# Kernel tuning notes

Measured on AMD Instinct MI355X. Metric: run time of the kernel, lower is better.

Reference implementation:

```python
import jax, jax.numpy as jnp
import numpy as np
from jax import lax

B, H, LQ, LF, V = 8, 12, 32, 256, 32000


def setup_inputs() -> dict:
    key = jax.random.key(0)
    k1, k2, k3 = jax.random.split(key, 3)
    return {
        "attention_scores": jax.random.normal(k1, (B, H, LQ, LF), jnp.float32),
        "q_logits": jax.random.normal(k2, (B, LQ, V), jnp.float32),
        "f_logits": jax.random.normal(k3, (B, LF, V), jnp.float32),
        "q_mask": jnp.ones((B, LQ), jnp.float32),
        "attention_mask": jnp.ones((B, LF), jnp.float32),
        "samples": 4,
    }


def reference(attention_scores, q_logits, f_logits, q_mask, attention_mask, samples):
    # attention_scores: [B,H,Lq,Lf] -> mean over heads, max over query positions
    scores = attention_scores.mean(axis=1)            # [B,Lq,Lf]
    aggregated = scores.max(axis=1)                   # [B,Lf]
    probs = jax.nn.sigmoid(aggregated) * attention_mask  # [B,Lf]

    # Bernoulli sampling for first samples-1 draws, deterministic threshold for the last
    skey = jax.random.key(42)
    sampled = jax.random.bernoulli(skey, probs, (samples - 1,) + probs.shape)
    last = (probs >= 0.5)[None]
    actions = jnp.concatenate([sampled, last], axis=0).astype(f_logits.dtype)  # [S,B,Lf]

    # Bernoulli log-prob summed over tokens: a*log(p) + (1-a)*log(1-p)
    logprobs = jnp.where(actions > 0.5, jnp.log(probs)[None], jnp.log1p(-probs)[None]).sum(-1)  # [S,B]

    # value = max over concat([q_logits, f_logits*action]) of log1p(relu(.)) * mask
    # Since action in {0,1}: log1p(relu(x*a)) = a * log1p(relu(x))
    lq = jnp.log1p(jax.nn.relu(q_logits)) * q_mask[:, :, None]   # [B,Lq,V]
    q_max = lq.max(axis=1)                                       # [B,V]
    lf = jnp.log1p(jax.nn.relu(f_logits))                        # [B,Lf,V]

    def step(carry, action):
        am = (action * attention_mask)[:, :, None]               # [B,Lf,1]
        f_val = (lf * am).max(axis=1)                            # [B,V]
        return carry, jnp.maximum(q_max, f_val)                  # masked max over concat dim

    _, values = lax.scan(step, None, actions)                    # [S,B,V]
    return values, logprobs, actions
```

## Files before the change

### kernel.cpp

```cpp
#include <hip/hip_runtime.h>
#include <stdint.h>

#define NB 8
#define NH 12
#define NLQ 32
#define NLF 256
#define NV 32000
#define NS 4
#define NV4 (NV / 4)

#define OUT_LOGP (NS * NB * NV)
#define OUT_ACT  (OUT_LOGP + NS * NB)

__device__ __forceinline__ uint32_t rotl32(uint32_t v, int r) {
  return (v << r) | (v >> (32 - r));
}

__device__ __forceinline__ void threefry2x32(uint32_t k0, uint32_t k1,
                                             uint32_t& x0, uint32_t& x1) {
  const uint32_t ks2 = k0 ^ k1 ^ 0x1BD11BDAu;
  x0 += k0; x1 += k1;
#define TF_ROUND(r) { x0 += x1; x1 = rotl32(x1, r); x1 ^= x0; }
  TF_ROUND(13) TF_ROUND(15) TF_ROUND(26) TF_ROUND(6)
  x0 += k1; x1 += ks2 + 1u;
  TF_ROUND(17) TF_ROUND(29) TF_ROUND(16) TF_ROUND(24)
  x0 += ks2; x1 += k0 + 2u;
  TF_ROUND(13) TF_ROUND(15) TF_ROUND(26) TF_ROUND(6)
  x0 += k0; x1 += k1 + 3u;
  TF_ROUND(17) TF_ROUND(29) TF_ROUND(16) TF_ROUND(24)
  x0 += k1; x1 += ks2 + 4u;
  TF_ROUND(13) TF_ROUND(15) TF_ROUND(26) TF_ROUND(6)
  x0 += ks2; x1 += k0 + 5u;
#undef TF_ROUND
}

__global__ __launch_bounds__(256) void k_mean(const float* __restrict__ as,
                                              float* __restrict__ scores) {
  const int o = blockIdx.x * 256 + threadIdx.x;
  const int f  = o & (NLF - 1);
  const int lq = (o >> 8) & (NLQ - 1);
  const int b  = o >> 13;
  float s = 0.f;
#pragma unroll
  for (int h = 0; h < NH; ++h)
    s += as[(((size_t)(b * NH + h) * NLQ) + lq) * NLF + f];
  scores[o] = s / 12.0f;
}

__global__ __launch_bounds__(256) void k_probs(
    const float* __restrict__ scores,
    const float* __restrict__ attn_mask,
    float* __restrict__ out,
    unsigned* __restrict__ actmask)
{
  const int b = blockIdx.x;
  const int f = threadIdx.x;

  float agg = -INFINITY;
#pragma unroll
  for (int lq = 0; lq < NLQ; ++lq)
    agg = fmaxf(agg, scores[(b * NLQ + lq) * NLF + f]);

  const float amask = attn_mask[b * NLF + f];
  const float p = amask * (1.0f / (1.0f + expf(-agg)));

  const float lp  = logf(p);
  const float l1p = log1pf(-p);

  unsigned mask = 0;
  float terms[NS];
#pragma unroll
  for (int s = 0; s < NS; ++s) {
    bool act;
    if (s < NS - 1) {
      const uint32_t n = (uint32_t)(s * (NB * NLF) + b * NLF + f);
      uint32_t x0 = 0u, x1 = n;
      threefry2x32(0u, 42u, x0, x1);
      const uint32_t bits = x0 ^ x1;
      const float u = __uint_as_float((bits >> 9) | 0x3f800000u) - 1.0f;
      act = (u < p);
    } else {
      act = (p >= 0.5f);
    }
    if (act) mask |= (1u << s);
    terms[s] = act ? lp : l1p;
    out[OUT_ACT + (s * NB + b) * NLF + f] = act ? 1.0f : 0.0f;
  }
  actmask[b * NLF + f] = mask;

  __shared__ float red[NS][NLF];
#pragma unroll
  for (int s = 0; s < NS; ++s) red[s][f] = terms[s];
  __syncthreads();
  for (int off = 128; off > 0; off >>= 1) {
    if (f < off) {
#pragma unroll
      for (int s = 0; s < NS; ++s) red[s][f] += red[s][f + off];
    }
    __syncthreads();
  }
  if (f == 0) {
#pragma unroll
    for (int s = 0; s < NS; ++s) out[OUT_LOGP + s * NB + b] = red[s][0];
  }
}

__global__ __launch_bounds__(256) void k_values(
    const float* __restrict__ q_logits,
    const float* __restrict__ f_logits,
    const float* __restrict__ q_mask,
    const unsigned* __restrict__ actmask,
    float* __restrict__ out)
{
  const int b = blockIdx.y;
  const int tid = threadIdx.x;

  __shared__ float ssel[NS][NLF];
  __shared__ float sqsel[NLQ];
  {
    const unsigned mk = actmask[b * NLF + tid];
#pragma unroll
    for (int s = 0; s < NS; ++s)
      ssel[s][tid] = (mk >> s) & 1u ? INFINITY : -INFINITY;
    if (tid < NLQ)
      sqsel[tid] = (q_mask[b * NLQ + tid] > 0.5f) ? INFINITY : -INFINITY;
  }
  __syncthreads();

  const int c4 = blockIdx.x * 256 + tid;
  if (c4 >= NV4) return;

  const float4* qp = (const float4*)q_logits;
  const float4* fp = (const float4*)f_logits;

  float4 qm4 = make_float4(-INFINITY, -INFINITY, -INFINITY, -INFINITY);
#pragma unroll
  for (int l0 = 0; l0 < NLQ; l0 += 8) {
    float4 x[8];
#pragma unroll
    for (int j = 0; j < 8; ++j)
      x[j] = qp[(size_t)(b * NLQ + l0 + j) * NV4 + c4];
#pragma unroll
    for (int j = 0; j < 8; ++j) {
      const float sv = sqsel[l0 + j];
      qm4.x = fmaxf(qm4.x, fminf(x[j].x, sv));
      qm4.y = fmaxf(qm4.y, fminf(x[j].y, sv));
      qm4.z = fmaxf(qm4.z, fminf(x[j].z, sv));
      qm4.w = fmaxf(qm4.w, fminf(x[j].w, sv));
    }
  }
  const float q0 = log1pf(fmaxf(qm4.x, 0.f));
  const float q1 = log1pf(fmaxf(qm4.y, 0.f));
  const float q2 = log1pf(fmaxf(qm4.z, 0.f));
  const float q3 = log1pf(fmaxf(qm4.w, 0.f));

  float m[NS][4];
#pragma unroll
  for (int s = 0; s < NS; ++s)
#pragma unroll
    for (int c = 0; c < 4; ++c) m[s][c] = -INFINITY;

  for (int f0 = 0; f0 < NLF; f0 += 8) {
    float4 x[8];
#pragma unroll
    for (int j = 0; j < 8; ++j)
      x[j] = fp[(size_t)(b * NLF + f0 + j) * NV4 + c4];
#pragma unroll
    for (int j = 0; j < 8; ++j) {
#pragma unroll
      for (int s = 0; s < NS; ++s) {
        const float sv = ssel[s][f0 + j];
        m[s][0] = fmaxf(m[s][0], fminf(x[j].x, sv));
        m[s][1] = fmaxf(m[s][1], fminf(x[j].y, sv));
        m[s][2] = fmaxf(m[s][2], fminf(x[j].z, sv));
        m[s][3] = fmaxf(m[s][3], fminf(x[j].w, sv));
      }
    }
  }

  float4* ov = (float4*)out;
#pragma unroll
  for (int s = 0; s < NS; ++s) {
    float4 r;
    r.x = fmaxf(q0, log1pf(fmaxf(m[s][0], 0.f)));
    r.y = fmaxf(q1, log1pf(fmaxf(m[s][1], 0.f)));
    r.z = fmaxf(q2, log1pf(fmaxf(m[s][2], 0.f)));
    r.w = fmaxf(q3, log1pf(fmaxf(m[s][3], 0.f)));
    ov[(size_t)(s * NB + b) * NV4 + c4] = r;
  }
}

extern "C" void kernel_launch(void* const* d_in, const int* in_sizes, int n_in,
                              void* d_out, int out_size, void* d_ws, size_t ws_size,
                              hipStream_t stream) {
  const float* attn_scores = (const float*)d_in[0];
  const float* q_logits    = (const float*)d_in[1];
  const float* f_logits    = (const float*)d_in[2];
  const float* q_mask      = (const float*)d_in[3];
  const float* attn_mask   = (const float*)d_in[4];
  float* out = (float*)d_out;

  float* ws_scores   = (float*)d_ws;
  unsigned* ws_mask  = (unsigned*)(ws_scores + NB * NLQ * NLF);

  k_mean<<<dim3((NB * NLQ * NLF) / 256), 256, 0, stream>>>(attn_scores, ws_scores);
  k_probs<<<dim3(NB), 256, 0, stream>>>(ws_scores, attn_mask, out, ws_mask);
  k_values<<<dim3((NV4 + 255) / 256, NB), 256, 0, stream>>>(
      q_logits, f_logits, q_mask, ws_mask, out);
}
```

Before: 388.7 us.

## Split the values reduction over token chunks and add a finalize max kernel

Splits the q/f token reduction in the values kernel into four chunks along a new grid dimension. Each chunk writes raw partial maxima to workspace, and a new finalize kernel combines them and applies log1p(relu). The goal is more blocks in flight to better saturate memory bandwidth. The cost is extra workspace traffic for the partials and one more kernel launch.

Result: slower. 396.9 us (+2.1%).

```diff
diff --git a/kernel.cpp b/kernel.cpp
--- a/kernel.cpp
+++ b/kernel.cpp
@@ -8,6 +8,10 @@
 #define NV 32000
 #define NS 4
 #define NV4 (NV / 4)
+
+#define PSPLIT 4
+#define FCHUNK (NLF / PSPLIT)
+#define QCHUNK (NLQ / PSPLIT)
 
 #define OUT_LOGP (NS * NB * NV)
 #define OUT_ACT  (OUT_LOGP + NS * NB)
@@ -105,26 +109,28 @@
   }
 }
 
-__global__ __launch_bounds__(256) void k_values(
+__global__ __launch_bounds__(256) void k_values_part(
     const float* __restrict__ q_logits,
     const float* __restrict__ f_logits,
     const float* __restrict__ q_mask,
     const unsigned* __restrict__ actmask,
-    float* __restrict__ out)
+    float* __restrict__ part)
 {
   const int b = blockIdx.y;
+  const int p = blockIdx.z;
   const int tid = threadIdx.x;
 
-  __shared__ float ssel[NS][NLF];
-  __shared__ float sqsel[NLQ];
-  {
-    const unsigned mk = actmask[b * NLF + tid];
+  __shared__ float ssel[NS][FCHUNK];
+  __shared__ float sqsel[QCHUNK];
+  if (tid < FCHUNK) {
+    const unsigned mk = actmask[b * NLF + p * FCHUNK + tid];
 #pragma unroll
     for (int s = 0; s < NS; ++s)
       ssel[s][tid] = (mk >> s) & 1u ? INFINITY : -INFINITY;
-    if (tid < NLQ)
-      sqsel[tid] = (q_mask[b * NLQ + tid] > 0.5f) ? INFINITY : -INFINITY;
-  }
+  }
+  if (tid < QCHUNK)
+    sqsel[tid] = (q_mask[b * NLQ + p * QCHUNK + tid] > 0.5f) ? INFINITY
+                                                             : -INFINITY;
   __syncthreads();
 
   const int c4 = blockIdx.x * 256 + tid;
@@ -133,38 +139,37 @@
   const float4* qp = (const float4*)q_logits;
   const float4* fp = (const float4*)f_logits;
 
-  float4 qm4 = make_float4(-INFINITY, -INFINITY, -INFINITY, -INFINITY);
-#pragma unroll
-  for (int l0 = 0; l0 < NLQ; l0 += 8) {
+  float m[NS][4];
+#pragma unroll
+  for (int s = 0; s < NS; ++s)
+#pragma unroll
+    for (int c = 0; c < 4; ++c) m[s][c] = -INFINITY;
+
+  {
     float4 x[8];
 #pragma unroll
     for (int j = 0; j < 8; ++j)
-      x[j] = qp[(size_t)(b * NLQ + l0 + j) * NV4 + c4];
+      x[j] = qp[(size_t)(b * NLQ + p * QCHUNK + j) * NV4 + c4];
+    float qm[4] = {-INFINITY, -INFINITY, -INFINITY, -INFINITY};
 #pragma unroll
     for (int j = 0; j < 8; ++j) {
-      const float sv = sqsel[l0 + j];
-      qm4.x = fmaxf(qm4.x, fminf(x[j].x, sv));
-      qm4.y = fmaxf(qm4.y, fminf(x[j].y, sv));
-      qm4.z = fmaxf(qm4.z, fminf(x[j].z, sv));
-      qm4.w = fmaxf(qm4.w, fminf(x[j].w, sv));
-    }
-  }
-  const float q0 = log1pf(fmaxf(qm4.x, 0.f));
-  const float q1 = log1pf(fmaxf(qm4.y, 0.f));
-  const float q2 = log1pf(fmaxf(qm4.z, 0.f));
-  const float q3 = log1pf(fmaxf(qm4.w, 0.f));
-
-  float m[NS][4];
-#pragma unroll
-  for (int s = 0; s < NS; ++s)
-#pragma unroll
-    for (int c = 0; c < 4; ++c) m[s][c] = -INFINITY;
-
-  for (int f0 = 0; f0 < NLF; f0 += 8) {
+      const float sv = sqsel[j];
+      qm[0] = fmaxf(qm[0], fminf(x[j].x, sv));
+      qm[1] = fmaxf(qm[1], fminf(x[j].y, sv));
+      qm[2] = fmaxf(qm[2], fminf(x[j].z, sv));
+      qm[3] = fmaxf(qm[3], fminf(x[j].w, sv));
+    }
+#pragma unroll
+    for (int s = 0; s < NS; ++s)
+#pragma unroll
+      for (int c = 0; c < 4; ++c) m[s][c] = fmaxf(m[s][c], qm[c]);
+  }
+
+  for (int f0 = 0; f0 < FCHUNK; f0 += 8) {
     float4 x[8];
 #pragma unroll
     for (int j = 0; j < 8; ++j)
-      x[j] = fp[(size_t)(b * NLF + f0 + j) * NV4 + c4];
+      x[j] = fp[(size_t)(b * NLF + p * FCHUNK + f0 + j) * NV4 + c4];
 #pragma unroll
     for (int j = 0; j < 8; ++j) {
 #pragma unroll
@@ -178,14 +183,49 @@
     }
   }
 
-  float4* ov = (float4*)out;
+  float4* pp = (float4*)part;
 #pragma unroll
   for (int s = 0; s < NS; ++s) {
     float4 r;
-    r.x = fmaxf(q0, log1pf(fmaxf(m[s][0], 0.f)));
-    r.y = fmaxf(q1, log1pf(fmaxf(m[s][1], 0.f)));
-    r.z = fmaxf(q2, log1pf(fmaxf(m[s][2], 0.f)));
-    r.w = fmaxf(q3, log1pf(fmaxf(m[s][3], 0.f)));
+    r.x = m[s][0]; r.y = m[s][1]; r.z = m[s][2]; r.w = m[s][3];
+    pp[((size_t)(p * NS + s) * NB + b) * NV4 + c4] = r;
+  }
+}
+
+__global__ __launch_bounds__(256) void k_finalize(
+    const float* __restrict__ part,
+    float* __restrict__ out)
+{
+  const int b = blockIdx.y;
+  const int tid = threadIdx.x;
+  const int c4 = blockIdx.x * 256 + tid;
+  if (c4 >= NV4) return;
+
+  const float4* pp = (const float4*)part;
+  float4* ov = (float4*)out;
+
+  float4 t[PSPLIT][NS];
+#pragma unroll
+  for (int p = 0; p < PSPLIT; ++p)
+#pragma unroll
+    for (int s = 0; s < NS; ++s)
+      t[p][s] = pp[((size_t)(p * NS + s) * NB + b) * NV4 + c4];
+
+#pragma unroll
+  for (int s = 0; s < NS; ++s) {
+    float4 mm = t[0][s];
+#pragma unroll
+    for (int p = 1; p < PSPLIT; ++p) {
+      mm.x = fmaxf(mm.x, t[p][s].x);
+      mm.y = fmaxf(mm.y, t[p][s].y);
+      mm.z = fmaxf(mm.z, t[p][s].z);
+      mm.w = fmaxf(mm.w, t[p][s].w);
+    }
+    float4 r;
+    r.x = log1pf(fmaxf(mm.x, 0.f));
+    r.y = log1pf(fmaxf(mm.y, 0.f));
+    r.z = log1pf(fmaxf(mm.z, 0.f));
+    r.w = log1pf(fmaxf(mm.w, 0.f));
     ov[(size_t)(s * NB + b) * NV4 + c4] = r;
   }
 }
@@ -202,9 +242,11 @@
 
   float* ws_scores   = (float*)d_ws;
   unsigned* ws_mask  = (unsigned*)(ws_scores + NB * NLQ * NLF);
+  float* ws_part     = (float*)(ws_mask + NB * NLF);
 
   k_mean<<<dim3((NB * NLQ * NLF) / 256), 256, 0, stream>>>(attn_scores, ws_scores);
   k_probs<<<dim3(NB), 256, 0, stream>>>(ws_scores, attn_mask, out, ws_mask);
-  k_values<<<dim3((NV4 + 255) / 256, NB), 256, 0, stream>>>(
-      q_logits, f_logits, q_mask, ws_mask, out);
-}
+  k_values_part<<<dim3((NV4 + 255) / 256, NB, PSPLIT), 256, 0, stream>>>(
+      q_logits, f_logits, q_mask, ws_mask, ws_part);
+  k_finalize<<<dim3((NV4 + 255) / 256, NB), 256, 0, stream>>>(ws_part, out);
+}
```

## Split LF reduction across four thread groups per block with shared-memory combine

Applied to the files above, without the earlier changes.

The values kernel now launches 1024 threads per block, and each group of 256 threads reduces a quarter of the f_logits rows and a quarter of the q_logits rows. Partial maxima go through shared memory and are combined by the first group, which applies log1p once to the merged max. The goal is more memory-level parallelism: the grid is only about 256 blocks, so per-thread serial streaming over 256 rows limits bandwidth use. The cost is 48KB of shared memory for the reduction buffer, a block barrier, and possible limits on occupancy from register pressure at 1024 threads.

Measured after the change: 392.4 us. About the same (+1.0%).

```diff
diff --git a/kernel.cpp b/kernel.cpp
--- a/kernel.cpp
+++ b/kernel.cpp
@@ -8,6 +8,10 @@
 #define NV 32000
 #define NS 4
 #define NV4 (NV / 4)
+
+#define NPART 4
+#define FCHUNK (NLF / NPART)
+#define QCHUNK (NLQ / NPART)
 
 #define OUT_LOGP (NS * NB * NV)
 #define OUT_ACT  (OUT_LOGP + NS * NB)
@@ -105,7 +109,7 @@
   }
 }
 
-__global__ __launch_bounds__(256) void k_values(
+__global__ __launch_bounds__(1024) void k_values(
     const float* __restrict__ q_logits,
     const float* __restrict__ f_logits,
     const float* __restrict__ q_mask,
@@ -114,62 +118,64 @@
 {
   const int b = blockIdx.y;
   const int tid = threadIdx.x;
+  const int lane_c = tid & 255;
+  const int part = tid >> 8;
 
   __shared__ float ssel[NS][NLF];
   __shared__ float sqsel[NLQ];
-  {
+  __shared__ float4 red[NPART - 1][256][NS];
+  if (tid < NLF) {
     const unsigned mk = actmask[b * NLF + tid];
 #pragma unroll
     for (int s = 0; s < NS; ++s)
       ssel[s][tid] = (mk >> s) & 1u ? INFINITY : -INFINITY;
-    if (tid < NLQ)
-      sqsel[tid] = (q_mask[b * NLQ + tid] > 0.5f) ? INFINITY : -INFINITY;
-  }
+  }
+  if (tid < NLQ)
+    sqsel[tid] = (q_mask[b * NLQ + tid] > 0.5f) ? INFINITY : -INFINITY;
   __syncthreads();
 
-  const int c4 = blockIdx.x * 256 + tid;
-  if (c4 >= NV4) return;
+  const int c4r = blockIdx.x * 256 + lane_c;
+  const int c4 = (c4r < NV4) ? c4r : (NV4 - 1);
 
   const float4* qp = (const float4*)q_logits;
   const float4* fp = (const float4*)f_logits;
 
-  float4 qm4 = make_float4(-INFINITY, -INFINITY, -INFINITY, -INFINITY);
-#pragma unroll
-  for (int l0 = 0; l0 < NLQ; l0 += 8) {
+  float m[NS][4];
+#pragma unroll
+  for (int s = 0; s < NS; ++s)
+#pragma unroll
+    for (int c = 0; c < 4; ++c) m[s][c] = -INFINITY;
+
+  {
     float4 x[8];
 #pragma unroll
     for (int j = 0; j < 8; ++j)
-      x[j] = qp[(size_t)(b * NLQ + l0 + j) * NV4 + c4];
+      x[j] = qp[(size_t)(b * NLQ + part * QCHUNK + j) * NV4 + c4];
+    float qm[4] = {-INFINITY, -INFINITY, -INFINITY, -INFINITY};
 #pragma unroll
     for (int j = 0; j < 8; ++j) {
-      const float sv = sqsel[l0 + j];
-      qm4.x = fmaxf(qm4.x, fminf(x[j].x, sv));
-      qm4.y = fmaxf(qm4.y, fminf(x[j].y, sv));
-      qm4.z = fmaxf(qm4.z, fminf(x[j].z, sv));
-      qm4.w = fmaxf(qm4.w, fminf(x[j].w, sv));
-    }
-  }
-  const float q0 = log1pf(fmaxf(qm4.x, 0.f));
-  const float q1 = log1pf(fmaxf(qm4.y, 0.f));
-  const float q2 = log1pf(fmaxf(qm4.z, 0.f));
-  const float q3 = log1pf(fmaxf(qm4.w, 0.f));
-
-  float m[NS][4];
-#pragma unroll
-  for (int s = 0; s < NS; ++s)
-#pragma unroll
-    for (int c = 0; c < 4; ++c) m[s][c] = -INFINITY;
-
-  for (int f0 = 0; f0 < NLF; f0 += 8) {
+      const float sv = sqsel[part * QCHUNK + j];
+      qm[0] = fmaxf(qm[0], fminf(x[j].x, sv));
+      qm[1] = fmaxf(qm[1], fminf(x[j].y, sv));
+      qm[2] = fmaxf(qm[2], fminf(x[j].z, sv));
+      qm[3] = fmaxf(qm[3], fminf(x[j].w, sv));
+    }
+#pragma unroll
+    for (int s = 0; s < NS; ++s)
+#pragma unroll
+      for (int c = 0; c < 4; ++c) m[s][c] = fmaxf(m[s][c], qm[c]);
+  }
+
+  for (int f0 = 0; f0 < FCHUNK; f0 += 8) {
     float4 x[8];
 #pragma unroll
     for (int j = 0; j < 8; ++j)
-      x[j] = fp[(size_t)(b * NLF + f0 + j) * NV4 + c4];
+      x[j] = fp[(size_t)(b * NLF + part * FCHUNK + f0 + j) * NV4 + c4];
 #pragma unroll
     for (int j = 0; j < 8; ++j) {
 #pragma unroll
       for (int s = 0; s < NS; ++s) {
-        const float sv = ssel[s][f0 + j];
+        const float sv = ssel[s][part * FCHUNK + f0 + j];
         m[s][0] = fmaxf(m[s][0], fminf(x[j].x, sv));
         m[s][1] = fmaxf(m[s][1], fminf(x[j].y, sv));
         m[s][2] = fmaxf(m[s][2], fminf(x[j].z, sv));
@@ -178,15 +184,33 @@
     }
   }
 
-  float4* ov = (float4*)out;
-#pragma unroll
-  for (int s = 0; s < NS; ++s) {
-    float4 r;
-    r.x = fmaxf(q0, log1pf(fmaxf(m[s][0], 0.f)));
-    r.y = fmaxf(q1, log1pf(fmaxf(m[s][1], 0.f)));
-    r.z = fmaxf(q2, log1pf(fmaxf(m[s][2], 0.f)));
-    r.w = fmaxf(q3, log1pf(fmaxf(m[s][3], 0.f)));
-    ov[(size_t)(s * NB + b) * NV4 + c4] = r;
+  if (part != 0) {
+#pragma unroll
+    for (int s = 0; s < NS; ++s)
+      red[part - 1][lane_c][s] = make_float4(m[s][0], m[s][1], m[s][2], m[s][3]);
+  }
+  __syncthreads();
+
+  if (part == 0 && c4r < NV4) {
+    float4* ov = (float4*)out;
+#pragma unroll
+    for (int s = 0; s < NS; ++s) {
+      float4 mm = make_float4(m[s][0], m[s][1], m[s][2], m[s][3]);
+#pragma unroll
+      for (int p = 0; p < NPART - 1; ++p) {
+        const float4 t = red[p][lane_c][s];
+        mm.x = fmaxf(mm.x, t.x);
+        mm.y = fmaxf(mm.y, t.y);
+        mm.z = fmaxf(mm.z, t.z);
+        mm.w = fmaxf(mm.w, t.w);
+      }
+      float4 r;
+      r.x = log1pf(fmaxf(mm.x, 0.f));
+      r.y = log1pf(fmaxf(mm.y, 0.f));
+      r.z = log1pf(fmaxf(mm.z, 0.f));
+      r.w = log1pf(fmaxf(mm.w, 0.f));
+      ov[(size_t)(s * NB + b) * NV4 + c4r] = r;
+    }
   }
 }
 
@@ -205,6 +229,6 @@
 
   k_mean<<<dim3((NB * NLQ * NLF) / 256), 256, 0, stream>>>(attn_scores, ws_scores);
   k_probs<<<dim3(NB), 256, 0, stream>>>(ws_scores, attn_mask, out, ws_mask);
-  k_values<<<dim3((NV4 + 255) / 256, NB), 256, 0, stream>>>(
+  k_values<<<dim3((NV4 + 255) / 256, NB), 1024, 0, stream>>>(
       q_logits, f_logits, q_mask, ws_mask, out);
 }
```

## Fuse probs/sampling into values kernel, recompute per block, use nontemporal loads

Applied to the files above, without the earlier changes.

Merges the probability/sampling kernel into the values kernel. Every block recomputes the per-batch probabilities, the threefry samples and the selection masks, while only the first column block writes actions and logprobs. This drops one launch and the actmask workspace round-trip, at the cost of redundant sigmoid/threefry work in each of the 32x8 blocks. It also widens the load batch from 8 to 16 rows and switches to nontemporal loads and stores for the streamed logits and outputs.

After: 362.3 us. -6.8%, faster.

```diff
diff --git a/kernel.cpp b/kernel.cpp
--- a/kernel.cpp
+++ b/kernel.cpp
@@ -11,6 +11,9 @@
 
 #define OUT_LOGP (NS * NB * NV)
 #define OUT_ACT  (OUT_LOGP + NS * NB)
+
+
+typedef float f32x4 __attribute__((ext_vector_type(4)));
 
 __device__ __forceinline__ uint32_t rotl32(uint32_t v, int r) {
   return (v << r) | (v >> (32 - r));
@@ -47,14 +50,21 @@
   scores[o] = s / 12.0f;
 }
 
-__global__ __launch_bounds__(256) void k_probs(
+__global__ __launch_bounds__(256, 1) void k_fused(
     const float* __restrict__ scores,
     const float* __restrict__ attn_mask,
-    float* __restrict__ out,
-    unsigned* __restrict__ actmask)
+    const float* __restrict__ q_logits,
+    const float* __restrict__ f_logits,
+    const float* __restrict__ q_mask,
+    float* __restrict__ out)
 {
-  const int b = blockIdx.x;
-  const int f = threadIdx.x;
+  const int b  = blockIdx.y;
+  const int cx = blockIdx.x;
+  const int f  = threadIdx.x;
+
+  __shared__ float ssel[NS][NLF];
+  __shared__ float sqsel[NLQ];
+  __shared__ float red[NS][NLF];
 
   float agg = -INFINITY;
 #pragma unroll
@@ -63,11 +73,9 @@
 
   const float amask = attn_mask[b * NLF + f];
   const float p = amask * (1.0f / (1.0f + expf(-agg)));
-
   const float lp  = logf(p);
   const float l1p = log1pf(-p);
 
-  unsigned mask = 0;
   float terms[NS];
 #pragma unroll
   for (int s = 0; s < NS; ++s) {
@@ -82,111 +90,88 @@
     } else {
       act = (p >= 0.5f);
     }
-    if (act) mask |= (1u << s);
+    ssel[s][f] = act ? INFINITY : -INFINITY;
     terms[s] = act ? lp : l1p;
-    out[OUT_ACT + (s * NB + b) * NLF + f] = act ? 1.0f : 0.0f;
+    if (cx == 0) out[OUT_ACT + (s * NB + b) * NLF + f] = act ? 1.0f : 0.0f;
   }
-  actmask[b * NLF + f] = mask;
-
-  __shared__ float red[NS][NLF];
+  if (f < NLQ)
+    sqsel[f] = (q_mask[b * NLQ + f] > 0.5f) ? INFINITY : -INFINITY;
+  if (cx == 0) {
 #pragma unroll
-  for (int s = 0; s < NS; ++s) red[s][f] = terms[s];
-  __syncthreads();
-  for (int off = 128; off > 0; off >>= 1) {
-    if (f < off) {
-#pragma unroll
-      for (int s = 0; s < NS; ++s) red[s][f] += red[s][f + off];
-    }
-    __syncthreads();
-  }
-  if (f == 0) {
-#pragma unroll
-    for (int s = 0; s < NS; ++s) out[OUT_LOGP + s * NB + b] = red[s][0];
-  }
-}
-
-__global__ __launch_bounds__(256) void k_values(
-    const float* __restrict__ q_logits,
-    const float* __restrict__ f_logits,
-    const float* __restrict__ q_mask,
-    const unsigned* __restrict__ actmask,
-    float* __restrict__ out)
-{
-  const int b = blockIdx.y;
-  const int tid = threadIdx.x;
-
-  __shared__ float ssel[NS][NLF];
-  __shared__ float sqsel[NLQ];
-  {
-    const unsigned mk = actmask[b * NLF + tid];
-#pragma unroll
-    for (int s = 0; s < NS; ++s)
-      ssel[s][tid] = (mk >> s) & 1u ? INFINITY : -INFINITY;
-    if (tid < NLQ)
-      sqsel[tid] = (q_mask[b * NLQ + tid] > 0.5f) ? INFINITY : -INFINITY;
+    for (int s = 0; s < NS; ++s) red[s][f] = terms[s];
   }
   __syncthreads();
 
-  const int c4 = blockIdx.x * 256 + tid;
+  if (cx == 0) {
+    for (int off = 128; off > 0; off >>= 1) {
+      if (f < off) {
+#pragma unroll
+        for (int s = 0; s < NS; ++s) red[s][f] += red[s][f + off];
+      }
+      __syncthreads();
+    }
+    if (f == 0) {
+#pragma unroll
+      for (int s = 0; s < NS; ++s) out[OUT_LOGP + s * NB + b] = red[s][0];
+    }
+  }
+
+  const int c4 = cx * 256 + f;
   if (c4 >= NV4) return;
 
-  const float4* qp = (const float4*)q_logits;
-  const float4* fp = (const float4*)f_logits;
+  const f32x4* qp = (const f32x4*)q_logits;
+  const f32x4* fp = (const f32x4*)f_logits;
+  const f32x4 NEGINF4 = {-INFINITY, -INFINITY, -INFINITY, -INFINITY};
 
-  float4 qm4 = make_float4(-INFINITY, -INFINITY, -INFINITY, -INFINITY);
+  f32x4 qm = NEGINF4;
+  for (int l0 = 0; l0 < NLQ; l0 += 16) {
+    f32x4 x[16];
 #pragma unroll
-  for (int l0 = 0; l0 < NLQ; l0 += 8) {
-    float4 x[8];
+    for (int j = 0; j < 16; ++j)
+      x[j] = __builtin_nontemporal_load(
+          &qp[(size_t)(b * NLQ + l0 + j) * NV4 + c4]);
 #pragma unroll
-    for (int j = 0; j < 8; ++j)
-      x[j] = qp[(size_t)(b * NLQ + l0 + j) * NV4 + c4];
+    for (int j = 0; j < 16; ++j) {
+      const float sv = sqsel[l0 + j];
 #pragma unroll
-    for (int j = 0; j < 8; ++j) {
-      const float sv = sqsel[l0 + j];
-      qm4.x = fmaxf(qm4.x, fminf(x[j].x, sv));
-      qm4.y = fmaxf(qm4.y, fminf(x[j].y, sv));
-      qm4.z = fmaxf(qm4.z, fminf(x[j].z, sv));
-      qm4.w = fmaxf(qm4.w, fminf(x[j].w, sv));
+      for (int c = 0; c < 4; ++c)
+        qm[c] = fmaxf(qm[c], fminf(x[j][c], sv));
     }
   }
-  const float q0 = log1pf(fmaxf(qm4.x, 0.f));
-  const float q1 = log1pf(fmaxf(qm4.y, 0.f));
-  const float q2 = log1pf(fmaxf(qm4.z, 0.f));
-  const float q3 = log1pf(fmaxf(qm4.w, 0.f));
+  float qlog[4];
+#pragma unroll
+  for (int c = 0; c < 4; ++c) qlog[c] = log1pf(fmaxf(qm[c], 0.f));
 
-  float m[NS][4];
+  f32x4 m[NS];
 #pragma unroll
-  for (int s = 0; s < NS; ++s)
+  for (int s = 0; s < NS; ++s) m[s] = NEGINF4;
+
+  for (int f0 = 0; f0 < NLF; f0 += 16) {
+    f32x4 x[16];
 #pragma unroll
-    for (int c = 0; c < 4; ++c) m[s][c] = -INFINITY;
-
-  for (int f0 = 0; f0 < NLF; f0 += 8) {
-    float4 x[8];
+    for (int j = 0; j < 16; ++j)
+      x[j] = __builtin_nontemporal_load(
+          &fp[(size_t)(b * NLF + f0 + j) * NV4 + c4]);
 #pragma unroll
-    for (int j = 0; j < 8; ++j)
-      x[j] = fp[(size_t)(b * NLF + f0 + j) * NV4 + c4];
-#pragma unroll
-    for (int j = 0; j < 8; ++j) {
+    for (int j = 0; j < 16; ++j) {
 #pragma unroll
       for (int s = 0; s < NS; ++s) {
         const float sv = ssel[s][f0 + j];
-        m[s][0] = fmaxf(m[s][0], fminf(x[j].x, sv));
-        m[s][1] = fmaxf(m[s][1], fminf(x[j].y, sv));
-        m[s][2] = fmaxf(m[s][2], fminf(x[j].z, sv));
-        m[s][3] = fmaxf(m[s][3], fminf(x[j].w, sv));
+#pragma unroll
+        for (int c = 0; c < 4; ++c)
+          m[s][c] = fmaxf(m[s][c], fminf(x[j][c], sv));
       }
     }
   }
 
-  float4* ov = (float4*)out;
+  f32x4* ov = (f32x4*)out;
 #pragma unroll
   for (int s = 0; s < NS; ++s) {
-    float4 r;
-    r.x = fmaxf(q0, log1pf(fmaxf(m[s][0], 0.f)));
-    r.y = fmaxf(q1, log1pf(fmaxf(m[s][1], 0.f)));
-    r.z = fmaxf(q2, log1pf(fmaxf(m[s][2], 0.f)));
-    r.w = fmaxf(q3, log1pf(fmaxf(m[s][3], 0.f)));
-    ov[(size_t)(s * NB + b) * NV4 + c4] = r;
+    f32x4 r;
+#pragma unroll
+    for (int c = 0; c < 4; ++c)
+      r[c] = fmaxf(qlog[c], log1pf(fmaxf(m[s][c], 0.f)));
+    __builtin_nontemporal_store(r, &ov[(size_t)(s * NB + b) * NV4 + c4]);
   }
 }
 
@@ -200,11 +185,9 @@
   const float* attn_mask   = (const float*)d_in[4];
   float* out = (float*)d_out;
 
-  float* ws_scores   = (float*)d_ws;
-  unsigned* ws_mask  = (unsigned*)(ws_scores + NB * NLQ * NLF);
+  float* ws_scores = (float*)d_ws;
 
   k_mean<<<dim3((NB * NLQ * NLF) / 256), 256, 0, stream>>>(attn_scores, ws_scores);
-  k_probs<<<dim3(NB), 256, 0, stream>>>(ws_scores, attn_mask, out, ws_mask);
-  k_values<<<dim3((NV4 + 255) / 256, NB), 256, 0, stream>>>(
-      q_logits, f_logits, q_mask, ws_mask, out);
+  k_fused<<<dim3((NV4 + 255) / 256, NB), 256, 0, stream>>>(
+      ws_scores, attn_mask, q_logits, f_logits, q_mask, out);
 }
```
